# Optimization experiments

Hardware: AMD Instinct MI355X
Metric: run time of the kernel (lower is better)

## Reference

```python
import jax, jax.numpy as jnp
import numpy as np
import math

B, L, IN, OUT = 32, 2048, 182, 2
H, N2, NL = 256, 32, 4  # hidden_dim, d_state//2, num_layers


def setup_inputs() -> dict:
    key = jax.random.key(0)
    ks = jax.random.split(key, 12)
    neural_input = jax.random.normal(ks[0], (B, L, IN), jnp.float32)
    # input / output projections
    Win = jax.random.normal(ks[1], (IN, H), jnp.float32) / np.sqrt(IN)
    b_in = jnp.zeros((H,), jnp.float32)
    Wout = jax.random.normal(ks[2], (H, OUT), jnp.float32) / np.sqrt(H)
    b_out = jnp.zeros((OUT,), jnp.float32)
    # stacked per-layer S4D params
    C2 = jax.random.normal(ks[3], (NL, H, N2, 2), jnp.float32)  # view_as_real of complex C
    log_dt = jax.random.uniform(ks[4], (NL, H), jnp.float32) * (math.log(0.1) - math.log(0.001)) + math.log(0.001)
    log_A_real = jnp.full((NL, H, N2), math.log(0.5), jnp.float32)
    A_imag = math.pi * jnp.broadcast_to(jnp.arange(N2, dtype=jnp.float32), (NL, H, N2))
    D = jax.random.normal(ks[5], (NL, H), jnp.float32)
    Wglu = jax.random.normal(ks[6], (NL, 2 * H, H), jnp.float32) / np.sqrt(H)
    bglu = jnp.zeros((NL, 2 * H), jnp.float32)
    return {"neural_input": neural_input, "Win": Win, "b_in": b_in,
            "C2": C2, "log_dt": log_dt, "log_A_real": log_A_real, "A_imag": A_imag,
            "D": D, "Wglu": Wglu, "bglu": bglu, "Wout": Wout, "b_out": b_out}


def _s4d_kernel(C2, log_dt, log_A_real, A_imag, length):
    # dt: (H,), A: (H,N2) complex
    dt = jnp.exp(log_dt)
    A = -jnp.exp(log_A_real) + 1j * A_imag
    dtA = A * dt[:, None]                      # (H, N2)
    C = (C2[..., 0] + 1j * C2[..., 1]) * (jnp.exp(dtA) - 1.0) / A
    t = jnp.arange(length, dtype=jnp.float32)
    E = jnp.exp(dtA[..., None] * t)            # (H, N2, L) complex
    K = 2.0 * jnp.einsum('hn,hnl->hl', C, E).real  # (H, L)
    return K


def _s4d_layer(u, C2, log_dt, log_A_real, A_imag, D, Wg, bg):
    # u: (B, H, L)
    length = u.shape[-1]
    k = _s4d_kernel(C2, log_dt, log_A_real, A_imag, length)
    k_f = jnp.fft.rfft(k, n=2 * length)        # (H, L+1)
    u_f = jnp.fft.rfft(u, n=2 * length)        # (B, H, L+1)
    y = jnp.fft.irfft(u_f * k_f, n=2 * length)[..., :length]
    y = y + u * D[:, None]
    y = jax.nn.gelu(y, approximate=False)      # nn.GELU default (erf)
    z = jnp.einsum('oh,bhl->bol', Wg, y) + bg[None, :, None]  # Conv1d k=1
    a, g = jnp.split(z, 2, axis=1)             # GLU over channel dim
    return a * jax.nn.sigmoid(g)


def reference(neural_input, Win, b_in, C2, log_dt, log_A_real, A_imag, D, Wglu, bglu, Wout, b_out):
    # input projection: (B, L, IN) -> (B, H, L)
    x = (neural_input @ Win + b_in).transpose(0, 2, 1)
    for i in range(NL):
        x = _s4d_layer(x, C2[i], log_dt[i], log_A_real[i], A_imag[i], D[i], Wglu[i], bglu[i])
    x = x.transpose(0, 2, 1)                   # (B, L, H)
    return x @ Wout + b_out                    # (B, L, OUT)
```

## Files before the change

### kernel.cpp

```cpp
#include <hip/hip_runtime.h>
#include <math.h>

typedef unsigned short u16;
typedef __attribute__((ext_vector_type(2))) unsigned short ushort2_t;
typedef __attribute__((ext_vector_type(4))) unsigned short ushort4_t;
typedef __attribute__((ext_vector_type(8))) unsigned short ushort8_t;
typedef __attribute__((ext_vector_type(8))) short short8;
typedef __attribute__((ext_vector_type(4))) float f32x4;

constexpr int Bn = 32, Ln = 2048, IN_DIM = 182, OUT_DIM = 2;
constexpr int Hn = 256, N2n = 32, NLn = 4;
constexpr int Tn = 64, NCn = Ln / Tn;
constexpr int KP = 192;
constexpr int IPPAD = 200;

__device__ inline u16 f2bf(float f) {
  unsigned int u = __float_as_uint(f);
  u += 0x7fffu + ((u >> 16) & 1u);
  return (u16)(u >> 16);
}
__device__ inline float bf2f(u16 v) { return __uint_as_float(((unsigned int)v) << 16); }

__global__ __launch_bounds__(256) void k_prep(const float* __restrict__ C2,
                                              const float* __restrict__ log_dt,
                                              const float* __restrict__ log_A_real,
                                              const float* __restrict__ A_imag,
                                              const float* __restrict__ Dp,
                                              float* __restrict__ cAT,
                                              u16* __restrict__ Lm, u16* __restrict__ Em,
                                              u16* __restrict__ Fm) {
  __shared__ float sdr[32], sdi[32], sCr[32], sCi[32];
  __shared__ float tmp[32][65];
  __shared__ float part[4][64];
  __shared__ float kt[64];
  int lh = blockIdx.x;
  int tid = threadIdx.x;
  if (tid < 32) {
    int n = tid;
    int idx = lh * N2n + n;
    float dt = expf(log_dt[lh]);
    float Ar = -expf(log_A_real[idx]);
    float Ai = A_imag[idx];
    float dr = Ar * dt, di = Ai * dt;
    float ea = expf(dr);
    float ar = ea * cosf(di), ai = ea * sinf(di);
    float eT = expf(dr * 64.0f);
    cAT[idx * 2 + 0] = eT * cosf(di * 64.0f);
    cAT[idx * 2 + 1] = eT * sinf(di * 64.0f);
    float nr = ar - 1.0f, ni = ai;
    float inv = 1.0f / (Ar * Ar + Ai * Ai);
    float qr = (nr * Ar + ni * Ai) * inv;
    float qi = (ni * Ar - nr * Ai) * inv;
    float c2r = C2[idx * 2 + 0], c2i = C2[idx * 2 + 1];
    sdr[n] = dr; sdi[n] = di;
    sCr[n] = 2.0f * (c2r * qr - c2i * qi);
    sCi[n] = 2.0f * (c2r * qi + c2i * qr);
  }
  __syncthreads();
  {
    int n = tid >> 3, dq = tid & 7;
    float dr = sdr[n], di = sdi[n], Cr = sCr[n], Ci = sCi[n];
    float d0 = (float)(dq * 8);
    float e0 = expf(dr * d0);
    float pr = e0 * cosf(di * d0), pi = e0 * sinf(di * d0);
    float ea = expf(dr);
    float ar = ea * cosf(di), ai = ea * sinf(di);
#pragma unroll
    for (int j = 0; j < 8; j++) {
      tmp[n][dq * 8 + j] = Cr * pr - Ci * pi;
      float t = pr * ar - pi * ai;
      pi = pr * ai + pi * ar;
      pr = t;
    }
  }
  __syncthreads();
  {
    int d = tid & 63, q = tid >> 6;
    float s = 0.0f;
#pragma unroll
    for (int k = 0; k < 8; k++) s += tmp[q * 8 + k][d];
    part[q][d] = s;
  }
  __syncthreads();
  if (tid < 64) kt[tid] = part[0][tid] + part[1][tid] + part[2][tid] + part[3][tid];
  __syncthreads();
  {
    int row = tid >> 2, tq = (tid & 3) * 16;
    float Dh = Dp[lh];
    u16 vals[16];
    for (int j = 0; j < 16; j++) {
      int d = row - (tq + j);
      float v = 0.0f;
      if (d >= 0) { v = kt[d]; if (d == 0) v += Dh; }
      vals[j] = f2bf(v);
    }
    u16* dst = Lm + (size_t)lh * 4096 + row * 64 + tq;
    ushort8_t o0, o1;
    for (int j = 0; j < 8; j++) { o0[j] = vals[j]; o1[j] = vals[8 + j]; }
    *(ushort8_t*)dst = o0;
    *(ushort8_t*)(dst + 8) = o1;
  }
  {
    int row = tid >> 2, tq = (tid & 3) * 16;
    int n = row >> 1, im = row & 1;
    float dr = sdr[n], di = sdi[n];
    float p0 = (float)(48 - tq);
    float e0 = expf(dr * p0);
    float pr = e0 * cosf(di * p0), pi = e0 * sinf(di * p0);
    float ea = expf(dr);
    float ar = ea * cosf(di), ai = ea * sinf(di);
    u16 vals[16];
#pragma unroll
    for (int j = 15; j >= 0; j--) {
      vals[j] = f2bf(im ? pi : pr);
      float t = pr * ar - pi * ai;
      pi = pr * ai + pi * ar;
      pr = t;
    }
    u16* dst = Em + (size_t)lh * 4096 + row * 64 + tq;
    ushort8_t o0, o1;
    for (int j = 0; j < 8; j++) { o0[j] = vals[j]; o1[j] = vals[8 + j]; }
    *(ushort8_t*)dst = o0;
    *(ushort8_t*)(dst + 8) = o1;
  }
  {
    int n2 = tid & 31, tg = tid >> 5;
    float dr = sdr[n2], di = sdi[n2], Cr = sCr[n2], Ci = sCi[n2];
    float p0 = (float)(tg * 8 + 1);
    float e0 = expf(dr * p0);
    float pr = e0 * cosf(di * p0), pi = e0 * sinf(di * p0);
    float ea = expf(dr);
    float ar = ea * cosf(di), ai = ea * sinf(di);
#pragma unroll
    for (int j = 0; j < 8; j++) {
      float wr = Cr * pr - Ci * pi;
      float wi = Cr * pi + Ci * pr;
      ushort2_t o; o[0] = f2bf(wr); o[1] = f2bf(-wi);
      *(ushort2_t*)(Fm + (size_t)lh * 4096 + (tg * 8 + j) * 64 + n2 * 2) = o;
      float t = pr * ar - pi * ai;
      pi = pr * ai + pi * ar;
      pr = t;
    }
  }
}

__global__ void k_wf(const float* __restrict__ Wglu, u16* __restrict__ Wf) {
  int idx = blockIdx.x * blockDim.x + threadIdx.x;
  if (idx >= NLn * 2 * Hn * Hn) return;
  int k = idx & 255;
  int o = (idx >> 8) & 511;
  int l = idx >> 17;
  size_t off = (size_t)l * (32 * 8192) + (size_t)(o >> 4) * 8192
             + (size_t)(k >> 3) * 256 + (o & 15) * 16 + (k & 7) * 2;
  *(u16*)((char*)Wf + off) = f2bf(Wglu[idx]);
}

__global__ void k_wtin(const float* __restrict__ Win, u16* __restrict__ Wt) {
  int idx = blockIdx.x * blockDim.x + threadIdx.x;
  if (idx >= Hn * KP) return;
  int h = idx / KP, k = idx - h * KP;
  Wt[idx] = (k < IN_DIM) ? f2bf(Win[(size_t)k * Hn + h]) : (u16)0;
}

__global__ __launch_bounds__(256) void k_inproj(const float* __restrict__ nin,
                                                const u16* __restrict__ Wt,
                                                const float* __restrict__ b_in,
                                                u16* __restrict__ Xc) {
  __shared__ __align__(16) u16 at[128 * IPPAD];
  int tid = threadIdx.x;
  int bx = blockIdx.x;
  int nb = blockIdx.y;
  int m0 = bx * 128;
  for (int i = tid; i < 128 * (IPPAD - IN_DIM); i += 256) {
    int r = i / (IPPAD - IN_DIM), c = IN_DIM + i - r * (IPPAD - IN_DIM);
    at[r * IPPAD + c] = 0;
  }
  const float4* src = (const float4*)(nin + (size_t)m0 * IN_DIM);
  for (int i = tid; i < 128 * IN_DIM / 4; i += 256) {
    float4 v = src[i];
    int e0 = i * 4;
    int r = e0 / IN_DIM;
    int c = e0 - r * IN_DIM;
    float vv[4] = {v.x, v.y, v.z, v.w};
#pragma unroll
    for (int j = 0; j < 4; j++) {
      int rr = r, cc = c + j;
      if (cc >= IN_DIM) { rr++; cc -= IN_DIM; }
      at[rr * IPPAD + cc] = f2bf(vv[j]);
    }
  }
  __syncthreads();
  int lane = tid & 63, wave = tid >> 6;
  int wm = wave >> 1, wn = wave & 1;
  int l15 = lane & 15, l4 = lane >> 4;
  int h0 = nb * 128 + wn * 64;
  f32x4 acc[4][4] = {};
#pragma unroll
  for (int ks = 0; ks < 6; ks++) {
    int k0 = ks * 32 + l4 * 8;
    short8 a[4], bfr[4];
#pragma unroll
    for (int mt = 0; mt < 4; mt++)
      a[mt] = *(const short8*)&at[(wm * 64 + mt * 16 + l15) * IPPAD + k0];
#pragma unroll
    for (int nt = 0; nt < 4; nt++)
      bfr[nt] = *(const short8*)(Wt + (size_t)(h0 + nt * 16 + l15) * KP + k0);
#pragma unroll
    for (int mt = 0; mt < 4; mt++)
#pragma unroll
      for (int nt = 0; nt < 4; nt++)
        acc[mt][nt] = __builtin_amdgcn_mfma_f32_16x16x32_bf16(a[mt], bfr[nt], acc[mt][nt], 0, 0, 0);
  }
#pragma unroll
  for (int mt = 0; mt < 4; mt++) {
#pragma unroll
    for (int nt = 0; nt < 4; nt++) {
      int j = h0 + nt * 16 + l15;
      float bb = b_in[j];
      int r0 = m0 + wm * 64 + mt * 16 + l4 * 4;
      int b = r0 >> 11, li = r0 & 2047;
      int c = li >> 6, t0 = li & 63;
      ushort4_t w;
#pragma unroll
      for (int r = 0; r < 4; r++) w[r] = f2bf(acc[mt][nt][r] + bb);
      *(ushort4_t*)(Xc + ((size_t)(b * NCn + c) * Hn + j) * Tn + t0) = w;
    }
  }
}

__global__ __launch_bounds__(512, 6) void k_s4d(const u16* __restrict__ Xc,
                                                const u16* __restrict__ Lm,
                                                const u16* __restrict__ Em,
                                                const u16* __restrict__ Fm,
                                                const float* __restrict__ cAT,
                                                u16* __restrict__ Gf, int layer) {
  __shared__ __align__(16) char sbuf[32768];
  __shared__ __align__(16) char ybuf[16384];
  int tid = threadIdx.x;
  int lane = tid & 63, w = tid >> 6;
  int l15 = lane & 15, l4 = lane >> 4;
  int flat = blockIdx.x;
  int vid = (flat & 7) * 128 + (flat >> 3);
  int hg = vid >> 5;
  int b = vid & 31;
  int h = hg * 8 + w;

  short8 ufr[2][2];
  const u16* xb = Xc + ((size_t)(b * NCn) * Hn + h) * Tn;
#pragma unroll
  for (int nt = 0; nt < 2; nt++)
#pragma unroll
    for (int ks = 0; ks < 2; ks++)
      ufr[nt][ks] = *(const short8*)(xb + (size_t)(nt * 16 + l15) * (Hn * Tn) + ks * 32 + l4 * 8);
  const u16* eb = Em + (size_t)(layer * Hn + h) * 4096;
#pragma unroll
  for (int mt = 0; mt < 4; mt++) {
    f32x4 sacc[2] = {};
#pragma unroll
    for (int ks = 0; ks < 2; ks++) {
      short8 af = *(const short8*)(eb + (mt * 16 + l15) * 64 + ks * 32 + l4 * 8);
#pragma unroll
      for (int nt = 0; nt < 2; nt++)
        sacc[nt] = __builtin_amdgcn_mfma_f32_16x16x32_bf16(af, ufr[nt][ks], sacc[nt], 0, 0, 0);
    }
    int comp0 = mt * 16 + l4 * 4;
    int g = comp0 >> 3, half = (comp0 >> 2) & 1;
#pragma unroll
    for (int nt = 0; nt < 2; nt++) {
      int c = nt * 16 + l15;
      ushort4_t wv;
#pragma unroll
      for (int r = 0; r < 4; r++) wv[r] = f2bf(sacc[nt][r]);
      *(ushort4_t*)(sbuf + w * 4096 + c * 128 + ((g ^ (c & 7)) << 4) + half * 8) = wv;
    }
  }
  __syncthreads();
  if (tid < 256) {
    int hl = tid >> 5, n = tid & 31;
    int hh = hg * 8 + hl;
    float aTr = cAT[((size_t)(layer * Hn + hh) * N2n + n) * 2 + 0];
    float aTi = cAT[((size_t)(layer * Hn + hh) * N2n + n) * 2 + 1];
    int grp = n >> 2, off = (n & 3) * 4;
    char* base = sbuf + hl * 4096;
    float cr = 0.0f, ci = 0.0f;
#pragma unroll
    for (int p = 0; p < 4; p++) {
      unsigned int sv[8];
#pragma unroll
      for (int q = 0; q < 8; q++) {
        int c = p * 8 + q;
        sv[q] = *(const unsigned int*)(base + c * 128 + ((grp ^ (c & 7)) << 4) + off);
      }
#pragma unroll
      for (int q = 0; q < 8; q++) {
        unsigned int s = sv[q];
        float sre = bf2f((u16)(s & 0xffffu));
        float sim = bf2f((u16)(s >> 16));
        sv[q] = (unsigned int)f2bf(cr) | ((unsigned int)f2bf(ci) << 16);
        float nr = aTr * cr - aTi * ci + sre;
        float ni = aTr * ci + aTi * cr + sim;
        cr = nr; ci = ni;
      }
#pragma unroll
      for (int q = 0; q < 8; q++) {
        int c = p * 8 + q;
        *(unsigned int*)(base + c * 128 + ((grp ^ (c & 7)) << 4) + off) = sv[q];
      }
    }
  }
  __syncthreads();
  const u16* lb = Lm + (size_t)(layer * Hn + h) * 4096;
  const u16* fb = Fm + (size_t)(layer * Hn + h) * 4096;
  u16* gp = Gf + (size_t)(hg * Bn + b) * Ln * 8;
  for (int nt = 0; nt < 2; nt++) {
    int c = nt * 16 + l15;
#pragma unroll
    for (int mt = 0; mt < 4; mt++) {
      f32x4 yacc = {};
#pragma unroll
      for (int ks = 0; ks < 2; ks++) {
        short8 af = *(const short8*)(lb + (mt * 16 + l15) * 64 + ks * 32 + l4 * 8);
        yacc = __builtin_amdgcn_mfma_f32_16x16x32_bf16(af, ufr[nt][ks], yacc, 0, 0, 0);
      }
#pragma unroll
      for (int ks = 0; ks < 2; ks++) {
        short8 af = *(const short8*)(fb + (mt * 16 + l15) * 64 + ks * 32 + l4 * 8);
        short8 bf = *(const short8*)(sbuf + w * 4096 + c * 128 + (((ks * 4 + l4) ^ (c & 7)) << 4));
        yacc = __builtin_amdgcn_mfma_f32_16x16x32_bf16(af, bf, yacc, 0, 0, 0);
      }
      int t0 = mt * 16 + l4 * 4;
      ushort4_t wv;
#pragma unroll
      for (int r = 0; r < 4; r++) {
        float y = yacc[r];
        wv[r] = f2bf(0.5f * y * (1.0f + erff(y * 0.70710678118654752f)));
      }
      int g = ((t0 >> 2) ^ l15) & 15;
      *(ushort4_t*)(ybuf + (l15 * 8 + w) * 128 + g * 8) = wv;
    }
    __syncthreads();
#pragma unroll
    for (int it = 0; it < 2; it++) {
      int mloc = it * 512 + tid;
      int cl = mloc >> 6, t = mloc & 63;
      int g = ((t >> 2) ^ cl) & 15;
      const char* bb = ybuf + (cl * 8) * 128 + g * 8 + (t & 3) * 2;
      ushort8_t o;
#pragma unroll
      for (int hl = 0; hl < 8; hl++) o[hl] = *(const u16*)(bb + hl * 128);
      int m = (nt * 16 + cl) * 64 + t;
      *(ushort8_t*)(gp + (size_t)m * 8) = o;
    }
    __syncthreads();
  }
}

template <int LAST>
__global__ __launch_bounds__(256) void k_glu(const u16* __restrict__ Gf,
                                             const u16* __restrict__ Wf,
                                             const float* __restrict__ bglu,
                                             u16* __restrict__ Xout, int layer) {
  int tid = threadIdx.x;
  int flat = blockIdx.x;
  int vid = (flat & 7) * 256 + (flat >> 3);
  int bx = vid >> 2;
  int nb = vid & 3;
  int lane = tid & 63, wave = tid >> 6;
  int wm = wave >> 1, wn = wave & 1;
  int l15 = lane & 15, l4 = lane >> 4;
  int m0 = bx * 128 + wm * 64;
  const char* wb = (const char*)Wf + (size_t)layer * 262144 + lane * 16;
  f32x4 acc[4][4] = {};
#pragma unroll 2
  for (int ks = 0; ks < 8; ks++) {
    short8 a[4], bfr[4];
#pragma unroll
    for (int rg = 0; rg < 4; rg++)
      a[rg] = *(const short8*)(Gf + (size_t)(ks * 4 + l4) * 524288 + (size_t)(m0 + rg * 16 + l15) * 8);
#pragma unroll
    for (int ct = 0; ct < 2; ct++) {
      bfr[ct]     = *(const short8*)(wb + (size_t)(nb * 4 + wn * 2 + ct) * 8192 + ks * 1024);
      bfr[ct + 2] = *(const short8*)(wb + (size_t)(16 + nb * 4 + wn * 2 + ct) * 8192 + ks * 1024);
    }
#pragma unroll
    for (int rg = 0; rg < 4; rg++)
#pragma unroll
      for (int ct = 0; ct < 4; ct++)
        acc[rg][ct] = __builtin_amdgcn_mfma_f32_16x16x32_bf16(a[rg], bfr[ct], acc[rg][ct], 0, 0, 0);
  }
  int c0 = nb * 64 + wn * 32;
#pragma unroll
  for (int rg = 0; rg < 4; rg++) {
#pragma unroll
    for (int ct = 0; ct < 2; ct++) {
      int j = c0 + ct * 16 + l15;
      float ba = bglu[layer * 512 + j];
      float bg = bglu[layer * 512 + 256 + j];
      f32x4 va = acc[rg][ct], vg = acc[rg][ct + 2];
      int r0 = m0 + rg * 16 + l4 * 4;
      if (LAST) {
#pragma unroll
        for (int r = 0; r < 4; r++) {
          float za = va[r] + ba, zg = vg[r] + bg;
          Xout[(size_t)(r0 + r) * Hn + j] = f2bf(za / (1.0f + expf(-zg)));
        }
      } else {
        int b = r0 >> 11, li = r0 & 2047;
        int c = li >> 6, t0 = li & 63;
        ushort4_t w;
#pragma unroll
        for (int r = 0; r < 4; r++) {
          float za = va[r] + ba, zg = vg[r] + bg;
          w[r] = f2bf(za / (1.0f + expf(-zg)));
        }
        *(ushort4_t*)(Xout + ((size_t)(b * NCn + c) * Hn + j) * Tn + t0) = w;
      }
    }
  }
}

__global__ __launch_bounds__(256) void k_outproj(const u16* __restrict__ Xp,
                                                 const float* __restrict__ Wout,
                                                 const float* __restrict__ b_out,
                                                 float* __restrict__ out) {
  int row = blockIdx.x * 4 + (threadIdx.x >> 6);
  int lane = threadIdx.x & 63;
  ushort4_t xv = *(const ushort4_t*)(Xp + (size_t)row * Hn + lane * 4);
  float x0 = bf2f(xv[0]), x1 = bf2f(xv[1]), x2 = bf2f(xv[2]), x3 = bf2f(xv[3]);
  const float4 w01 = *(const float4*)&Wout[lane * 8];
  const float4 w23 = *(const float4*)&Wout[lane * 8 + 4];
  float p0 = x0 * w01.x + x1 * w01.z + x2 * w23.x + x3 * w23.z;
  float p1 = x0 * w01.y + x1 * w01.w + x2 * w23.y + x3 * w23.w;
  for (int off = 32; off; off >>= 1) {
    p0 += __shfl_down(p0, off, 64);
    p1 += __shfl_down(p1, off, 64);
  }
  if (lane == 0) {
    out[(size_t)row * 2 + 0] = p0 + b_out[0];
    out[(size_t)row * 2 + 1] = p1 + b_out[1];
  }
}

extern "C" void kernel_launch(void* const* d_in, const int* in_sizes, int n_in,
                              void* d_out, int out_size, void* d_ws, size_t ws_size,
                              hipStream_t stream) {
  const float* nin        = (const float*)d_in[0];
  const float* Win        = (const float*)d_in[1];
  const float* b_in       = (const float*)d_in[2];
  const float* C2         = (const float*)d_in[3];
  const float* log_dt     = (const float*)d_in[4];
  const float* log_A_real = (const float*)d_in[5];
  const float* A_imag     = (const float*)d_in[6];
  const float* Dp         = (const float*)d_in[7];
  const float* Wglu       = (const float*)d_in[8];
  const float* bglu       = (const float*)d_in[9];
  const float* Wout       = (const float*)d_in[10];
  const float* b_out      = (const float*)d_in[11];
  float* out = (float*)d_out;

  u16* Xc = (u16*)d_ws;
  u16* Gf = Xc + (size_t)16777216;
  u16* Wt = Gf + (size_t)16777216;
  u16* Wf = Wt + (size_t)49152;
  u16* Lm = Wf + (size_t)524288;
  u16* Em = Lm + (size_t)4194304;
  u16* Fm = Em + (size_t)4194304;
  float* cAT = (float*)(Fm + (size_t)4194304);

  k_prep<<<NLn * Hn, 256, 0, stream>>>(C2, log_dt, log_A_real, A_imag, Dp, cAT, Lm, Em, Fm);
  k_wf<<<(NLn * 2 * Hn * Hn + 255) / 256, 256, 0, stream>>>(Wglu, Wf);
  k_wtin<<<(Hn * KP + 255) / 256, 256, 0, stream>>>(Win, Wt);
  k_inproj<<<dim3(512, 2), 256, 0, stream>>>(nin, Wt, b_in, Xc);
  for (int l = 0; l < NLn; l++) {
    k_s4d<<<1024, 512, 0, stream>>>(Xc, Lm, Em, Fm, cAT, Gf, l);
    if (l < NLn - 1)
      k_glu<0><<<2048, 256, 0, stream>>>(Gf, Wf, bglu, Xc, l);
    else
      k_glu<1><<<2048, 256, 0, stream>>>(Gf, Wf, bglu, Xc, l);
  }
  k_outproj<<<Bn * Ln / 4, 256, 0, stream>>>(Xc, Wout, b_out, out);
}
```

Measured before the change: 496.5 us.

## Shrink S4D shared memory, widen GLU and inproj blocks, vectorize weight prep

The S4D kernel drops its separate y buffer and reuses the state buffer, with the chunk operands pulled into registers before a barrier. This lowers LDS use so the launch bound can be raised to 8 blocks per CU. The GLU and input-projection kernels move to 512-thread blocks that cover more output columns per block, so activation tiles are reused across more waves. The input-projection LDS tile uses an XOR swizzle in place of padding, and k_wf converts weights with vectorized float4 loads. The extra barrier and the tighter register budget could cause spills.

```diff
diff --git a/kernel.cpp b/kernel.cpp
--- a/kernel.cpp
+++ b/kernel.cpp
@@ -12,7 +12,6 @@
 constexpr int Hn = 256, N2n = 32, NLn = 4;
 constexpr int Tn = 64, NCn = Ln / Tn;
 constexpr int KP = 192;
-constexpr int IPPAD = 200;
 
 __device__ inline u16 f2bf(float f) {
   unsigned int u = __float_as_uint(f);
@@ -145,14 +144,19 @@
 }
 
 __global__ void k_wf(const float* __restrict__ Wglu, u16* __restrict__ Wf) {
-  int idx = blockIdx.x * blockDim.x + threadIdx.x;
-  if (idx >= NLn * 2 * Hn * Hn) return;
-  int k = idx & 255;
-  int o = (idx >> 8) & 511;
-  int l = idx >> 17;
-  size_t off = (size_t)l * (32 * 8192) + (size_t)(o >> 4) * 8192
-             + (size_t)(k >> 3) * 256 + (o & 15) * 16 + (k & 7) * 2;
-  *(u16*)((char*)Wf + off) = f2bf(Wglu[idx]);
+  int tid = blockIdx.x * 256 + threadIdx.x;
+  int o15 = tid & 15;
+  int kg  = (tid >> 4) & 31;
+  int ot  = (tid >> 9) & 31;
+  int l   = tid >> 14;
+  int o = ot * 16 + o15;
+  const float* src = Wglu + ((size_t)(l * 512 + o) * 256 + kg * 8);
+  float4 f0 = *(const float4*)src;
+  float4 f1 = *(const float4*)(src + 4);
+  ushort8_t v;
+  v[0] = f2bf(f0.x); v[1] = f2bf(f0.y); v[2] = f2bf(f0.z); v[3] = f2bf(f0.w);
+  v[4] = f2bf(f1.x); v[5] = f2bf(f1.y); v[6] = f2bf(f1.z); v[7] = f2bf(f1.w);
+  *(ushort8_t*)((char*)Wf + (size_t)l * 262144 + ot * 8192 + kg * 256 + o15 * 16) = v;
 }
 
 __global__ void k_wtin(const float* __restrict__ Win, u16* __restrict__ Wt) {
@@ -162,21 +166,20 @@
   Wt[idx] = (k < IN_DIM) ? f2bf(Win[(size_t)k * Hn + h]) : (u16)0;
 }
 
-__global__ __launch_bounds__(256) void k_inproj(const float* __restrict__ nin,
+__global__ __launch_bounds__(512) void k_inproj(const float* __restrict__ nin,
                                                 const u16* __restrict__ Wt,
                                                 const float* __restrict__ b_in,
                                                 u16* __restrict__ Xc) {
-  __shared__ __align__(16) u16 at[128 * IPPAD];
+  __shared__ __align__(16) u16 at[128 * 192];
   int tid = threadIdx.x;
   int bx = blockIdx.x;
-  int nb = blockIdx.y;
   int m0 = bx * 128;
-  for (int i = tid; i < 128 * (IPPAD - IN_DIM); i += 256) {
-    int r = i / (IPPAD - IN_DIM), c = IN_DIM + i - r * (IPPAD - IN_DIM);
-    at[r * IPPAD + c] = 0;
+  for (int i = tid; i < 128 * 10; i += 512) {
+    int r = i / 10, k = IN_DIM + (i - r * 10);
+    *(u16*)((char*)at + r * 384 + ((((k >> 3)) ^ (r & 7)) << 4) + (k & 7) * 2) = 0;
   }
   const float4* src = (const float4*)(nin + (size_t)m0 * IN_DIM);
-  for (int i = tid; i < 128 * IN_DIM / 4; i += 256) {
+  for (int i = tid; i < 128 * IN_DIM / 4; i += 512) {
     float4 v = src[i];
     int e0 = i * 4;
     int r = e0 / IN_DIM;
@@ -186,22 +189,25 @@
     for (int j = 0; j < 4; j++) {
       int rr = r, cc = c + j;
       if (cc >= IN_DIM) { rr++; cc -= IN_DIM; }
-      at[rr * IPPAD + cc] = f2bf(vv[j]);
+      *(u16*)((char*)at + rr * 384 + ((((cc >> 3)) ^ (rr & 7)) << 4) + (cc & 7) * 2) = f2bf(vv[j]);
     }
   }
   __syncthreads();
   int lane = tid & 63, wave = tid >> 6;
-  int wm = wave >> 1, wn = wave & 1;
+  int wm = wave >> 2, wn = wave & 3;
   int l15 = lane & 15, l4 = lane >> 4;
-  int h0 = nb * 128 + wn * 64;
+  int h0 = wn * 64;
   f32x4 acc[4][4] = {};
 #pragma unroll
   for (int ks = 0; ks < 6; ks++) {
     int k0 = ks * 32 + l4 * 8;
+    int kg = ks * 4 + l4;
     short8 a[4], bfr[4];
 #pragma unroll
-    for (int mt = 0; mt < 4; mt++)
-      a[mt] = *(const short8*)&at[(wm * 64 + mt * 16 + l15) * IPPAD + k0];
+    for (int mt = 0; mt < 4; mt++) {
+      int row = wm * 64 + mt * 16 + l15;
+      a[mt] = *(const short8*)((const char*)at + row * 384 + ((kg ^ (row & 7)) << 4));
+    }
 #pragma unroll
     for (int nt = 0; nt < 4; nt++)
       bfr[nt] = *(const short8*)(Wt + (size_t)(h0 + nt * 16 + l15) * KP + k0);
@@ -228,14 +234,13 @@
   }
 }
 
-__global__ __launch_bounds__(512, 6) void k_s4d(const u16* __restrict__ Xc,
+__global__ __launch_bounds__(512, 8) void k_s4d(const u16* __restrict__ Xc,
                                                 const u16* __restrict__ Lm,
                                                 const u16* __restrict__ Em,
                                                 const u16* __restrict__ Fm,
                                                 const float* __restrict__ cAT,
                                                 u16* __restrict__ Gf, int layer) {
   __shared__ __align__(16) char sbuf[32768];
-  __shared__ __align__(16) char ybuf[16384];
   int tid = threadIdx.x;
   int lane = tid & 63, w = tid >> 6;
   int l15 = lane & 15, l4 = lane >> 4;
@@ -263,15 +268,14 @@
       for (int nt = 0; nt < 2; nt++)
         sacc[nt] = __builtin_amdgcn_mfma_f32_16x16x32_bf16(af, ufr[nt][ks], sacc[nt], 0, 0, 0);
     }
-    int comp0 = mt * 16 + l4 * 4;
-    int g = comp0 >> 3, half = (comp0 >> 2) & 1;
+    int g = mt * 2 + (l4 >> 1), half = l4 & 1;
 #pragma unroll
     for (int nt = 0; nt < 2; nt++) {
       int c = nt * 16 + l15;
       ushort4_t wv;
 #pragma unroll
       for (int r = 0; r < 4; r++) wv[r] = f2bf(sacc[nt][r]);
-      *(ushort4_t*)(sbuf + w * 4096 + c * 128 + ((g ^ (c & 7)) << 4) + half * 8) = wv;
+      *(ushort4_t*)(sbuf + nt * 16384 + w * 2048 + l15 * 128 + ((g ^ (c & 7)) << 4) + half * 8) = wv;
     }
   }
   __syncthreads();
@@ -281,7 +285,6 @@
     float aTr = cAT[((size_t)(layer * Hn + hh) * N2n + n) * 2 + 0];
     float aTi = cAT[((size_t)(layer * Hn + hh) * N2n + n) * 2 + 1];
     int grp = n >> 2, off = (n & 3) * 4;
-    char* base = sbuf + hl * 4096;
     float cr = 0.0f, ci = 0.0f;
 #pragma unroll
     for (int p = 0; p < 4; p++) {
@@ -289,7 +292,8 @@
 #pragma unroll
       for (int q = 0; q < 8; q++) {
         int c = p * 8 + q;
-        sv[q] = *(const unsigned int*)(base + c * 128 + ((grp ^ (c & 7)) << 4) + off);
+        sv[q] = *(const unsigned int*)(sbuf + (c >> 4) * 16384 + hl * 2048 + (c & 15) * 128 +
+                                       ((grp ^ (c & 7)) << 4) + off);
       }
 #pragma unroll
       for (int q = 0; q < 8; q++) {
@@ -304,7 +308,8 @@
 #pragma unroll
       for (int q = 0; q < 8; q++) {
         int c = p * 8 + q;
-        *(unsigned int*)(base + c * 128 + ((grp ^ (c & 7)) << 4) + off) = sv[q];
+        *(unsigned int*)(sbuf + (c >> 4) * 16384 + hl * 2048 + (c & 15) * 128 +
+                         ((grp ^ (c & 7)) << 4) + off) = sv[q];
       }
     }
   }
@@ -314,6 +319,12 @@
   u16* gp = Gf + (size_t)(hg * Bn + b) * Ln * 8;
   for (int nt = 0; nt < 2; nt++) {
     int c = nt * 16 + l15;
+    short8 cf[2];
+#pragma unroll
+    for (int ks = 0; ks < 2; ks++)
+      cf[ks] = *(const short8*)(sbuf + nt * 16384 + w * 2048 + l15 * 128 +
+                                (((ks * 4 + l4) ^ (c & 7)) << 4));
+    __syncthreads();
 #pragma unroll
     for (int mt = 0; mt < 4; mt++) {
       f32x4 yacc = {};
@@ -325,18 +336,16 @@
 #pragma unroll
       for (int ks = 0; ks < 2; ks++) {
         short8 af = *(const short8*)(fb + (mt * 16 + l15) * 64 + ks * 32 + l4 * 8);
-        short8 bf = *(const short8*)(sbuf + w * 4096 + c * 128 + (((ks * 4 + l4) ^ (c & 7)) << 4));
-        yacc = __builtin_amdgcn_mfma_f32_16x16x32_bf16(af, bf, yacc, 0, 0, 0);
-      }
-      int t0 = mt * 16 + l4 * 4;
+        yacc = __builtin_amdgcn_mfma_f32_16x16x32_bf16(af, cf[ks], yacc, 0, 0, 0);
+      }
       ushort4_t wv;
 #pragma unroll
       for (int r = 0; r < 4; r++) {
         float y = yacc[r];
         wv[r] = f2bf(0.5f * y * (1.0f + erff(y * 0.70710678118654752f)));
       }
-      int g = ((t0 >> 2) ^ l15) & 15;
-      *(ushort4_t*)(ybuf + (l15 * 8 + w) * 128 + g * 8) = wv;
+      int g = ((mt * 4 + l4) ^ l15) & 15;
+      *(ushort4_t*)(sbuf + nt * 16384 + (l15 * 8 + w) * 128 + g * 8) = wv;
     }
     __syncthreads();
 #pragma unroll
@@ -344,7 +353,7 @@
       int mloc = it * 512 + tid;
       int cl = mloc >> 6, t = mloc & 63;
       int g = ((t >> 2) ^ cl) & 15;
-      const char* bb = ybuf + (cl * 8) * 128 + g * 8 + (t & 3) * 2;
+      const char* bb = sbuf + nt * 16384 + (cl * 8) * 128 + g * 8 + (t & 3) * 2;
       ushort8_t o;
 #pragma unroll
       for (int hl = 0; hl < 8; hl++) o[hl] = *(const u16*)(bb + hl * 128);
@@ -356,17 +365,17 @@
 }
 
 template <int LAST>
-__global__ __launch_bounds__(256) void k_glu(const u16* __restrict__ Gf,
+__global__ __launch_bounds__(512) void k_glu(const u16* __restrict__ Gf,
                                              const u16* __restrict__ Wf,
                                              const float* __restrict__ bglu,
                                              u16* __restrict__ Xout, int layer) {
   int tid = threadIdx.x;
   int flat = blockIdx.x;
-  int vid = (flat & 7) * 256 + (flat >> 3);
-  int bx = vid >> 2;
-  int nb = vid & 3;
+  int vid = (flat & 7) * 128 + (flat >> 3);
+  int bx = vid >> 1;
+  int nb2 = vid & 1;
   int lane = tid & 63, wave = tid >> 6;
-  int wm = wave >> 1, wn = wave & 1;
+  int wm = wave >> 2, wn = wave & 3;
   int l15 = lane & 15, l4 = lane >> 4;
   int m0 = bx * 128 + wm * 64;
   const char* wb = (const char*)Wf + (size_t)layer * 262144 + lane * 16;
@@ -379,8 +388,9 @@
       a[rg] = *(const short8*)(Gf + (size_t)(ks * 4 + l4) * 524288 + (size_t)(m0 + rg * 16 + l15) * 8);
 #pragma unroll
     for (int ct = 0; ct < 2; ct++) {
-      bfr[ct]     = *(const short8*)(wb + (size_t)(nb * 4 + wn * 2 + ct) * 8192 + ks * 1024);
-      bfr[ct + 2] = *(const short8*)(wb + (size_t)(16 + nb * 4 + wn * 2 + ct) * 8192 + ks * 1024);
+      int ot = nb2 * 8 + wn * 2 + ct;
+      bfr[ct]     = *(const short8*)(wb + (size_t)ot * 8192 + ks * 1024);
+      bfr[ct + 2] = *(const short8*)(wb + (size_t)(16 + ot) * 8192 + ks * 1024);
     }
 #pragma unroll
     for (int rg = 0; rg < 4; rg++)
@@ -388,7 +398,7 @@
       for (int ct = 0; ct < 4; ct++)
         acc[rg][ct] = __builtin_amdgcn_mfma_f32_16x16x32_bf16(a[rg], bfr[ct], acc[rg][ct], 0, 0, 0);
   }
-  int c0 = nb * 64 + wn * 32;
+  int c0 = nb2 * 128 + wn * 32;
 #pragma unroll
   for (int rg = 0; rg < 4; rg++) {
 #pragma unroll
@@ -468,15 +478,15 @@
   float* cAT = (float*)(Fm + (size_t)4194304);
 
   k_prep<<<NLn * Hn, 256, 0, stream>>>(C2, log_dt, log_A_real, A_imag, Dp, cAT, Lm, Em, Fm);
-  k_wf<<<(NLn * 2 * Hn * Hn + 255) / 256, 256, 0, stream>>>(Wglu, Wf);
+  k_wf<<<256, 256, 0, stream>>>(Wglu, Wf);
   k_wtin<<<(Hn * KP + 255) / 256, 256, 0, stream>>>(Win, Wt);
-  k_inproj<<<dim3(512, 2), 256, 0, stream>>>(nin, Wt, b_in, Xc);
+  k_inproj<<<512, 512, 0, stream>>>(nin, Wt, b_in, Xc);
   for (int l = 0; l < NLn; l++) {
     k_s4d<<<1024, 512, 0, stream>>>(Xc, Lm, Em, Fm, cAT, Gf, l);
     if (l < NLn - 1)
-      k_glu<0><<<2048, 256, 0, stream>>>(Gf, Wf, bglu, Xc, l);
+      k_glu<0><<<1024, 512, 0, stream>>>(Gf, Wf, bglu, Xc, l);
     else
-      k_glu<1><<<2048, 256, 0, stream>>>(Gf, Wf, bglu, Xc, l);
+      k_glu<1><<<1024, 512, 0, stream>>>(Gf, Wf, bglu, Xc, l);
   }
   k_outproj<<<Bn * Ln / 4, 256, 0, stream>>>(Xc, Wout, b_out, out);
 }
```

Result: faster. 451.5 us (-9.1%).
